# Optimization experiments

Measured on AMD Instinct MI355X. Metric: run time of the kernel, lower is better.

Reference implementation:

```python
import jax, jax.numpy as jnp
import numpy as np

NUM_HEADS = 12

def get_rel_pos(q_size, k_size, rel_pos):
    # q_size == k_size here; relative index = i - j + (k_size - 1)
    idx = jnp.arange(q_size)[:, None] - jnp.arange(k_size)[None, :] + (k_size - 1)
    return rel_pos[idx]  # (q_size, k_size, head_dim)


def setup_inputs() -> dict:
    key = jax.random.key(0)
    ks = jax.random.split(key, 7)
    B, H, W, C = 1, 64, 64, 768
    return {
        "x": jax.random.normal(ks[0], (B, H, W, C), jnp.float32),
        "w_qkv": jax.random.normal(ks[1], (C, 3 * C), jnp.float32) * 0.02,
        "b_qkv": jnp.zeros((3 * C,), jnp.float32),
        "w_o": jax.random.normal(ks[2], (C, C), jnp.float32) * 0.02,
        "b_o": jnp.zeros((C,), jnp.float32),
        "rel_pos_h": jax.random.normal(ks[3], (2 * H - 1, C // NUM_HEADS), jnp.float32) * 0.02,
        "rel_pos_w": jax.random.normal(ks[4], (2 * W - 1, C // NUM_HEADS), jnp.float32) * 0.02,
    }


def reference(x, w_qkv, b_qkv, w_o, b_o, rel_pos_h, rel_pos_w):
    B, H, W, C = x.shape
    NH = NUM_HEADS
    HD = C // NH
    scale = HD ** -0.5  # 0.125

    qkv = x @ w_qkv + b_qkv                                   # (B,H,W,3C)
    qkv = qkv.reshape(B, H * W, 3, NH, HD)
    qkv = jnp.transpose(qkv, (2, 0, 3, 1, 4)).reshape(3, B * NH, H * W, HD)
    q, k, v = qkv[0], qkv[1], qkv[2]                          # (B*NH, HW, HD)

    Rh = get_rel_pos(H, H, rel_pos_h)                         # (H,H,HD)
    Rw = get_rel_pos(W, W, rel_pos_w)                         # (W,W,HD)
    qr = q.reshape(B * NH, H, W, HD)
    rel_h = jnp.einsum('bhwc,hkc->bhwk', qr, Rh)              # (B*NH,H,W,H)
    rel_w = jnp.einsum('bhwc,wkc->bhwk', qr, Rw)              # (B*NH,H,W,W)

    attn = jnp.einsum('bmd,bnd->bmn', q, k) * scale           # (B*NH,HW,HW)
    attn = attn.reshape(B * NH, H, W, H, W)
    attn = attn + rel_h[:, :, :, :, None] + rel_w[:, :, :, None, :]
    attn = attn.reshape(B * NH, H * W, H * W)

    p = jax.nn.softmax(attn, axis=-1)
    o = jnp.einsum('bmn,bnd->bmd', p, v)                      # (B*NH,HW,HD)
    o = o.reshape(B, NH, H * W, HD)
    o = jnp.transpose(o, (0, 2, 1, 3)).reshape(B, H, W, C)    # heads concat in channel dim
    return o @ w_o + b_o
```

## Files before the change

### kernel.cpp

```cpp
#include <hip/hip_runtime.h>

#define DEVI __device__ __forceinline__
typedef unsigned short u16;
typedef unsigned int u32;
typedef __attribute__((ext_vector_type(4))) float f4v;
typedef __attribute__((ext_vector_type(8))) short bf8v;
typedef __attribute__((ext_vector_type(4))) u32  u32x4;
typedef __attribute__((ext_vector_type(2))) u32  u32x2;
typedef __attribute__((ext_vector_type(4))) u16  u16x4;

#define AS1 __attribute__((address_space(1)))
#define AS3 __attribute__((address_space(3)))

DEVI u16 f2bf(float x){ union{float f;u32 u;} c{x}; u32 r=(c.u+0x7FFFu+((c.u>>16)&1u))>>16; return (u16)r; }
DEVI float bf2f(u16 b){ union{u32 u;float f;} c{(u32)b<<16}; return c.f; }
DEVI f4v mfma32(bf8v a, bf8v b, f4v c){ return __builtin_amdgcn_mfma_f32_16x16x32_bf16(a,b,c,0,0,0); }
DEVI unsigned lds_off(const void* p){ return (unsigned)(unsigned long)(AS3 const void*)p; }
DEVI void glds16(const void* g, void* l){
  __builtin_amdgcn_global_load_lds((AS1 void*)g, (AS3 void*)l, 16, 0, 0);
}

static constexpr int NH = 12, HW = 4096, D = 64, C = 768;
static constexpr float LOG2E = 1.44269504f;

__global__ void qa_convx(const float* __restrict__ x, u16* __restrict__ xb, int n4){
  int i = blockIdx.x*256 + threadIdx.x;
  if(i >= n4) return;
  f4v v = ((const f4v*)x)[i];
  u16x4 o; for(int j=0;j<4;j++) o[j] = f2bf(v[j]);
  ((u16x4*)xb)[i] = o;
}

__global__ void qa_transp(const float* __restrict__ in, u16* __restrict__ out, int R, int Cc, int scale_k){
  __shared__ float tl[32][33];
  int t = threadIdx.x;
  int r0 = blockIdx.y*32, c0 = blockIdx.x*32;
  int tr = t>>3, tc = (t&7)*4;
  f4v v = *(const f4v*)&in[(r0+tr)*Cc + c0 + tc];
  for(int j=0;j<4;j++) tl[tr][tc+j] = v[j];
  __syncthreads();
  int oc = t>>3, orr = (t&7)*4;
  float sc = (scale_k && (c0+oc) >= 768 && (c0+oc) < 1536) ? 0.125f*LOG2E : 1.0f;
  u16x4 o; for(int j=0;j<4;j++) o[j] = f2bf(tl[orr+j][oc]*sc);
  *(u16x4*)&out[(c0+oc)*R + r0 + orr] = o;
}

__global__ __launch_bounds__(256,2) void qa_gemm_qkv(
    const u16* __restrict__ A, const u16* __restrict__ Bt, const float* __restrict__ bias,
    u16* __restrict__ qb, u16* __restrict__ kb, u16* __restrict__ vb){
  __shared__ u16 Al[128*32], Bl[128*32];
  const int t = threadIdx.x, lane = t&63, w = t>>6, c16 = lane&15, h4 = lane>>4;
  const int m0 = blockIdx.y*128, n0 = blockIdx.x*128;
  const int wr = w>>1, wc = w&1;
  f4v acc[4][4];
  for(int nt=0;nt<4;nt++){
    f4v bv;
    for(int r=0;r<4;r++){
      int col = n0 + wc*64 + nt*16 + 4*h4 + r;
      float b = bias[col];
      bv[r] = (col >= 768 && col < 1536) ? b*0.125f*LOG2E : b;
    }
    for(int mt=0;mt<4;mt++) acc[mt][nt] = bv;
  }
  for(int k0 = 0; k0 < 768; k0 += 32){
    __syncthreads();
    for(int i=0;i<2;i++){
      int off = i*4096 + w*1024 + lane*16;
      int row = off>>6, kk = (off&63)>>1;
      glds16(A  + (size_t)(m0+row)*768 + k0 + kk, (u16*)Al + i*2048 + w*512);
      glds16(Bt + (size_t)(n0+row)*768 + k0 + kk, (u16*)Bl + i*2048 + w*512);
    }
    __syncthreads();
    bf8v a[4], b[4];
    for(int mt=0;mt<4;mt++) a[mt] = *(const bf8v*)&Al[(wr*64+mt*16+c16)*32 + h4*8];
    for(int nt=0;nt<4;nt++) b[nt] = *(const bf8v*)&Bl[(wc*64+nt*16+c16)*32 + h4*8];
    for(int mt=0;mt<4;mt++) for(int nt=0;nt<4;nt++) acc[mt][nt] = mfma32(b[nt], a[mt], acc[mt][nt]);
  }
  for(int mt=0;mt<4;mt++){
    int row = m0 + wr*64 + mt*16 + c16;
    for(int nt=0;nt<4;nt++){
      int col0 = n0 + wc*64 + nt*16 + 4*h4;
      int which = col0/768, head = (col0>>6)%12, d0 = col0&63;
      u16* dst = which==0 ? qb : (which==1 ? kb : vb);
      u32x2 pk;
      asm("v_cvt_pk_bf16_f32 %0, %1, %2" : "=v"(pk[0]) : "v"(acc[mt][nt][0]), "v"(acc[mt][nt][1]));
      asm("v_cvt_pk_bf16_f32 %0, %1, %2" : "=v"(pk[1]) : "v"(acc[mt][nt][2]), "v"(acc[mt][nt][3]));
      *(u32x2*)&dst[((size_t)(head<<12)+row)*64 + d0] = pk;
    }
  }
}

__global__ __launch_bounds__(256) void qa_rel(
    const u16* __restrict__ qbuf, const float* __restrict__ rph, const float* __restrict__ rpw,
    u16* __restrict__ RHt, u16* __restrict__ RW){
  const int t = threadIdx.x, lane = t&63, w = t>>6, c16 = lane&15, h4 = lane>>4;
  const int qh = blockIdx.x, head = blockIdx.y;
  __shared__ u16 ql[64*72], hl[64*72], wl[128*72];
  {
    int row = t>>2, d0 = (t&3)*16;
    const u16* src = qbuf + ((size_t)(head<<12)+(qh<<6)+row)*64 + d0;
    *(u32x4*)&ql[row*72+d0]   = *(const u32x4*)src;
    *(u32x4*)&ql[row*72+d0+8] = *(const u32x4*)(src+8);
    for(int j=0;j<16;j++) hl[row*72+d0+j] = f2bf(rph[(qh+row)*64 + d0 + j]);
    int rw_r = t>>1, rd0 = (t&1)*32;
    for(int j=0;j<32;j++) wl[rw_r*72+rd0+j] = (rw_r<127) ? f2bf(rpw[rw_r*64+rd0+j]) : (u16)0;
  }
  __syncthreads();
  if(w < 2){
    bf8v a[2][2]; f4v acc[2][4] = {};
    for(int mt=0;mt<2;mt++) for(int ch=0;ch<2;ch++)
      a[mt][ch] = *(const bf8v*)&ql[(w*32+mt*16+c16)*72 + ch*32 + h4*8];
    for(int nt=0;nt<4;nt++) for(int ch=0;ch<2;ch++){
      bf8v b = *(const bf8v*)&hl[(nt*16+c16)*72 + ch*32 + h4*8];
      for(int mt=0;mt<2;mt++) acc[mt][nt] = mfma32(a[mt][ch], b, acc[mt][nt]);
    }
    for(int mt=0;mt<2;mt++) for(int nt=0;nt<4;nt++) for(int r=0;r<4;r++){
      int qw = w*32+mt*16+4*h4+r, c = nt*16+c16, kh = 63 - c;
      RHt[((size_t)(head*64+qh)*64+kh)*64 + qw] = f2bf(acc[mt][nt][r]*LOG2E);
    }
  } else {
    bf8v a[2][2]; f4v acc[2][8] = {};
    for(int mt=0;mt<2;mt++) for(int ch=0;ch<2;ch++)
      a[mt][ch] = *(const bf8v*)&ql[((w-2)*32+mt*16+c16)*72 + ch*32 + h4*8];
    for(int nt=0;nt<8;nt++) for(int ch=0;ch<2;ch++){
      bf8v b = *(const bf8v*)&wl[(nt*16+c16)*72 + ch*32 + h4*8];
      for(int mt=0;mt<2;mt++) acc[mt][nt] = mfma32(a[mt][ch], b, acc[mt][nt]);
    }
    for(int mt=0;mt<2;mt++) for(int nt=0;nt<8;nt++) for(int r=0;r<4;r++){
      int qw = (w-2)*32+mt*16+4*h4+r, c = nt*16+c16, kw = qw + 63 - c;
      if((unsigned)kw < 64u) RW[((size_t)(head*64+qh)*64+qw)*64 + kw] = f2bf(acc[mt][nt][r]*LOG2E);
    }
  }
}

__global__ __launch_bounds__(256,4) void qa_attn(
    const u16* __restrict__ qb, const u16* __restrict__ kb, const u16* __restrict__ vb,
    const u16* __restrict__ RHt, const u16* __restrict__ RW,
    u16* __restrict__ Op, float* __restrict__ Ps){
  __shared__ u16 Kl[2][4096];
  __shared__ u16 Vl[2][4096];
  __shared__ u16 RHl[2048];
  const int t = threadIdx.x, lane = t&63, w = t>>6, c16 = lane&15, h4 = lane>>4;
  const int bid = blockIdx.x;
  const int g = (bid&7)*192 + (bid>>3);
  const int s = g&1, unit = g>>1;
  const int head = unit>>6, qt = unit&63;

  const u16* rhg = RHt + (size_t)unit*4096 + s*2048;
  glds16(rhg + t*8, (u16*)RHl + w*512);

  int koff[2], voff[2];
  for(int i=0;i<2;i++){
    int u = i*256 + t;
    koff[i] = (u ^ ((u>>3)&7))*8;
    int key = ((u>>1)&3) | (((u>>3)&15)<<2);
    int d0  = ((u&1)<<3) | (((u>>7)&3)<<4);
    voff[i] = key*64 + d0;
  }
  const u16* kg = kb + (size_t)head*262144 + (size_t)s*32*4096;
  const u16* vg = vb + (size_t)head*262144 + (size_t)s*32*4096;
  const u16* kp = kg; const u16* vp = vg;
  for(int i=0;i<2;i++){
    glds16(kp + koff[i], (u16*)Kl[0] + (i*256 + w*64)*8);
    glds16(vp + voff[i], (u16*)Vl[0] + (i*256 + w*64)*8);
  }
  kp += 4096; vp += 4096;

  const int q0r = qt*64 + w*16;
  bf8v qa[2];
  {
    const u16* qsrc = qb + ((size_t)head*4096 + q0r + c16)*64;
    qa[0] = *(const bf8v*)(qsrc + h4*8);
    qa[1] = *(const bf8v*)(qsrc + 32 + h4*8);
  }
  float rw[4][4];
  for(int nt=0;nt<4;nt++) for(int r=0;r<4;r++){
    int qw = w*16 + c16, kw = nt*16 + 4*h4 + r;
    rw[nt][r] = bf2f(RW[((size_t)unit*64 + qw)*64 + kw]);
  }

  f4v oacc[4] = {}; f4v psv = {0.f,0.f,0.f,0.f};
  unsigned vcur = lds_off(Vl) + lane*8;
  const int kq0 = (h4*16) ^ ((c16&7)<<4);
  const int kq1 = (h4*16 + 64) ^ ((c16&7)<<4);
  const int kA  = c16*128;

  for(int it=0; it<32; it++){
    if(it == 31){ kp = kg; vp = vg; }
    {
      u16* Kn = (u16*)Kl[(it+1)&1]; u16* Vn = (u16*)Vl[(it+1)&1];
      for(int i=0;i<2;i++){
        glds16(kp + koff[i], Kn + (i*256 + w*64)*8);
        glds16(vp + voff[i], Vn + (i*256 + w*64)*8);
      }
    }
    kp += 4096; vp += 4096;
    asm volatile("s_waitcnt vmcnt(4)\n\ts_barrier" ::: "memory");

    const char* Kc = (const char*)Kl + (it&1)*8192;
    float rh = bf2f(RHl[it*64 + w*16 + c16]);
    f4v p[4];
    #pragma unroll
    for(int nt=0;nt<4;nt++){
      bf8v k0 = *(const bf8v*)(Kc + kA + nt*2048 + kq0);
      bf8v k1 = *(const bf8v*)(Kc + kA + nt*2048 + kq1);
      f4v sv;
      for(int r=0;r<4;r++) sv[r] = rh + rw[nt][r];
      __builtin_amdgcn_s_setprio(1);
      sv = mfma32(k0, qa[0], sv);
      sv = mfma32(k1, qa[1], sv);
      __builtin_amdgcn_s_setprio(0);
      f4v pe;
      for(int r=0;r<4;r++) pe[r] = __builtin_amdgcn_exp2f(sv[r]);
      p[nt] = pe;
      psv += pe;
    }
    union U8 { u32 w[4]; bf8v v; };
    U8 pb[2];
    #pragma unroll
    for(int half=0;half<2;half++)
      #pragma unroll
      for(int i=0;i<4;i++){
        int nt = half*2 + (i>>1), r0 = (i&1)*2;
        asm("v_cvt_pk_bf16_f32 %0, %1, %2"
            : "=v"(pb[half].w[i]) : "v"(p[nt][r0]), "v"(p[nt][r0+1]));
      }
    #pragma unroll
    for(int dt=0;dt<4;dt++){
      unsigned long t00,t01,t10,t11;
      asm volatile(
        "ds_read_b64_tr_b16 %0, %4 offset:%c5\n\t"
        "ds_read_b64_tr_b16 %1, %4 offset:%c6\n\t"
        "ds_read_b64_tr_b16 %2, %4 offset:%c7\n\t"
        "ds_read_b64_tr_b16 %3, %4 offset:%c8\n\t"
        "s_waitcnt lgkmcnt(0)"
        : "=&v"(t00), "=&v"(t01), "=&v"(t10), "=&v"(t11)
        : "v"(vcur), "i"(dt*2048), "i"(dt*2048+512), "i"(dt*2048+1024), "i"(dt*2048+1536)
        : "memory");
      union { struct{ unsigned long a,b; } q; bf8v v; } v01, v23;
      v01.q.a = t00; v01.q.b = t01; v23.q.a = t10; v23.q.b = t11;
      __builtin_amdgcn_s_setprio(1);
      oacc[dt] = mfma32(v01.v, pb[0].v, oacc[dt]);
      oacc[dt] = mfma32(v23.v, pb[1].v, oacc[dt]);
      __builtin_amdgcn_s_setprio(0);
    }
    asm volatile("s_waitcnt lgkmcnt(0)\n\ts_barrier" ::: "memory");
    vcur ^= 8192;
  }
  asm volatile("s_waitcnt vmcnt(0)" ::: "memory");

  {
    float v = psv[0]+psv[1]+psv[2]+psv[3];
    v += __shfl_xor(v, 16); v += __shfl_xor(v, 32);
    const int qrow_l = w*16 + c16;
    if(h4 == 0) Ps[((size_t)unit*2 + s)*64 + qrow_l] = v;
    const size_t obase = (((size_t)unit*2 + s)*64 + qrow_l)*64;
    #pragma unroll
    for(int dt=0;dt<4;dt++){
      u32x2 pk;
      asm("v_cvt_pk_bf16_f32 %0, %1, %2" : "=v"(pk[0]) : "v"(oacc[dt][0]), "v"(oacc[dt][1]));
      asm("v_cvt_pk_bf16_f32 %0, %1, %2" : "=v"(pk[1]) : "v"(oacc[dt][2]), "v"(oacc[dt][3]));
      *(u32x2*)&Op[obase + dt*16 + 4*h4] = pk;
    }
  }
}

__global__ __launch_bounds__(256) void qa_reduce(
    const u16* __restrict__ Op, const float* __restrict__ Ps, u16* __restrict__ ob){
  const int unit = blockIdx.x, t = threadIdx.x;
  const int head = unit>>6, qt = unit&63;
  const int d0 = (t&15)*4;
  #pragma unroll
  for(int qq=0;qq<4;qq++){
    int qr = (t>>4) + qq*16;
    float inv = 1.0f / (Ps[((size_t)unit*2)*64 + qr] + Ps[((size_t)unit*2+1)*64 + qr]);
    u16x4 a = *(const u16x4*)&Op[(((size_t)unit*2  )*64 + qr)*64 + d0];
    u16x4 b = *(const u16x4*)&Op[(((size_t)unit*2+1)*64 + qr)*64 + d0];
    u16x4 o;
    for(int j=0;j<4;j++) o[j] = f2bf((bf2f(a[j]) + bf2f(b[j]))*inv);
    *(u16x4*)&ob[(size_t)(qt*64 + qr)*768 + head*64 + d0] = o;
  }
}

__global__ __launch_bounds__(256,2) void qa_gemm_out(
    const u16* __restrict__ A, const u16* __restrict__ Bt, const float* __restrict__ bias,
    float* __restrict__ out){
  __shared__ u16 Al[128*32], Bl[128*32];
  const int t = threadIdx.x, lane = t&63, w = t>>6, c16 = lane&15, h4 = lane>>4;
  const int m0 = blockIdx.y*128, n0 = blockIdx.x*128;
  const int wr = w>>1, wc = w&1;
  f4v acc[4][4];
  for(int nt=0;nt<4;nt++){
    f4v bv = *(const f4v*)&bias[n0 + wc*64 + nt*16 + 4*h4];
    for(int mt=0;mt<4;mt++) acc[mt][nt] = bv;
  }
  for(int k0 = 0; k0 < 768; k0 += 32){
    __syncthreads();
    for(int i=0;i<2;i++){
      int off = i*4096 + w*1024 + lane*16;
      int row = off>>6, kk = (off&63)>>1;
      glds16(A  + (size_t)(m0+row)*768 + k0 + kk, (u16*)Al + i*2048 + w*512);
      glds16(Bt + (size_t)(n0+row)*768 + k0 + kk, (u16*)Bl + i*2048 + w*512);
    }
    __syncthreads();
    bf8v a[4], b[4];
    for(int mt=0;mt<4;mt++) a[mt] = *(const bf8v*)&Al[(wr*64+mt*16+c16)*32 + h4*8];
    for(int nt=0;nt<4;nt++) b[nt] = *(const bf8v*)&Bl[(wc*64+nt*16+c16)*32 + h4*8];
    for(int mt=0;mt<4;mt++) for(int nt=0;nt<4;nt++) acc[mt][nt] = mfma32(b[nt], a[mt], acc[mt][nt]);
  }
  for(int mt=0;mt<4;mt++){
    int row = m0 + wr*64 + mt*16 + c16;
    for(int nt=0;nt<4;nt++){
      int col0 = n0 + wc*64 + nt*16 + 4*h4;
      *(f4v*)&out[(size_t)row*768 + col0] = acc[mt][nt];
    }
  }
}

extern "C" void kernel_launch(void* const* d_in, const int* in_sizes, int n_in,
                              void* d_out, int out_size, void* d_ws, size_t ws_size,
                              hipStream_t stream){
  const float* x    = (const float*)d_in[0];
  const float* wqkv = (const float*)d_in[1];
  const float* bqkv = (const float*)d_in[2];
  const float* wo   = (const float*)d_in[3];
  const float* bo   = (const float*)d_in[4];
  const float* rph  = (const float*)d_in[5];
  const float* rpw  = (const float*)d_in[6];
  float* out = (float*)d_out;

  size_t off = 0;
  auto alloc = [&](size_t bytes){ void* p = (char*)d_ws + off; off += (bytes + 255) & ~(size_t)255; return p; };
  u16* x_bf   = (u16*)alloc((size_t)HW*C*2);
  u16* wqkv_t = (u16*)alloc((size_t)2304*768*2);
  u16* wo_t   = (u16*)alloc((size_t)768*768*2);
  u16* q_buf  = (u16*)alloc((size_t)NH*HW*D*2);
  u16* k_buf  = (u16*)alloc((size_t)NH*HW*D*2);
  u16* v_buf  = (u16*)alloc((size_t)NH*HW*D*2);
  u16* rh_buf = (u16*)alloc((size_t)NH*64*64*64*2);
  u16* rw_buf = (u16*)alloc((size_t)NH*64*64*64*2);
  u16* o_buf  = (u16*)alloc((size_t)HW*C*2);
  u16* op_buf = (u16*)alloc((size_t)768*2*64*64*2);
  float* ps_buf = (float*)alloc((size_t)768*2*64*4);

  int n4 = HW*C/4;
  qa_convx<<<(n4+255)/256, 256, 0, stream>>>(x, x_bf, n4);
  qa_transp<<<dim3(2304/32, 768/32), 256, 0, stream>>>(wqkv, wqkv_t, 768, 2304, 1);
  qa_transp<<<dim3(768/32, 768/32),  256, 0, stream>>>(wo,   wo_t,   768, 768, 0);
  qa_gemm_qkv<<<dim3(2304/128, HW/128), 256, 0, stream>>>(x_bf, wqkv_t, bqkv, q_buf, k_buf, v_buf);
  qa_rel<<<dim3(64, NH), 256, 0, stream>>>(q_buf, rph, rpw, rh_buf, rw_buf);
  qa_attn<<<1536, 256, 0, stream>>>(q_buf, k_buf, v_buf, rh_buf, rw_buf, op_buf, ps_buf);
  qa_reduce<<<768, 256, 0, stream>>>(op_buf, ps_buf, o_buf);
  qa_gemm_out<<<dim3(768/128, HW/128), 256, 0, stream>>>(o_buf, wo_t, bo, out);
}
```

Measured before the change: 154.9 us.

## Double the attention query tile to 128 rows per block

Each attention block now processes 128 query rows instead of 64, with every wave handling two 16-row query chunks against each shared K/V tile. This halves the K/V tile loads and barriers per unit of work and halves the grid size and partial-output buffers, with the reduce kernel adjusted to match. The cost is roughly double the accumulator and score registers per thread, so the occupancy target drops from 4 to 3 blocks per SM. There are also fewer blocks (768) to spread across the compute units.

New measurement: 144.1 us. -7.0%, faster.

```diff
diff --git a/kernel.cpp b/kernel.cpp
--- a/kernel.cpp
+++ b/kernel.cpp
@@ -133,32 +133,36 @@
   }
 }
 
-__global__ __launch_bounds__(256,4) void qa_attn(
+__global__ __launch_bounds__(256,3) void qa_attn(
     const u16* __restrict__ qb, const u16* __restrict__ kb, const u16* __restrict__ vb,
     const u16* __restrict__ RHt, const u16* __restrict__ RW,
     u16* __restrict__ Op, float* __restrict__ Ps){
   __shared__ u16 Kl[2][4096];
   __shared__ u16 Vl[2][4096];
-  __shared__ u16 RHl[2048];
+  __shared__ u16 RHl[4096];
   const int t = threadIdx.x, lane = t&63, w = t>>6, c16 = lane&15, h4 = lane>>4;
   const int bid = blockIdx.x;
-  const int g = (bid&7)*192 + (bid>>3);
-  const int s = g&1, unit = g>>1;
-  const int head = unit>>6, qt = unit&63;
-
-  const u16* rhg = RHt + (size_t)unit*4096 + s*2048;
-  glds16(rhg + t*8, (u16*)RHl + w*512);
+  const int g = (bid&7)*96 + (bid>>3);
+  const int s = g&1, u = g>>1;
+  const int head = u>>5, qblk = u&31;
+  const int B0 = qblk*128;
+  const int qhl = w>>1;
+
+  for(int i=0;i<2;i++){
+    const u16* rhsrc = RHt + (((size_t)(head*64 + qblk*2 + i))*64 + s*32)*64;
+    glds16(rhsrc + t*8, (u16*)RHl + i*2048 + w*512);
+  }
 
   int koff[2], voff[2];
   for(int i=0;i<2;i++){
-    int u = i*256 + t;
-    koff[i] = (u ^ ((u>>3)&7))*8;
-    int key = ((u>>1)&3) | (((u>>3)&15)<<2);
-    int d0  = ((u&1)<<3) | (((u>>7)&3)<<4);
+    int uu = i*256 + t;
+    koff[i] = (uu ^ ((uu>>3)&7))*8;
+    int key = ((uu>>1)&3) | (((uu>>3)&15)<<2);
+    int d0  = ((uu&1)<<3) | (((uu>>7)&3)<<4);
     voff[i] = key*64 + d0;
   }
-  const u16* kg = kb + (size_t)head*262144 + (size_t)s*32*4096;
-  const u16* vg = vb + (size_t)head*262144 + (size_t)s*32*4096;
+  const u16* kg = kb + (size_t)head*262144 + (size_t)s*131072;
+  const u16* vg = vb + (size_t)head*262144 + (size_t)s*131072;
   const u16* kp = kg; const u16* vp = vg;
   for(int i=0;i<2;i++){
     glds16(kp + koff[i], (u16*)Kl[0] + (i*256 + w*64)*8);
@@ -166,20 +170,20 @@
   }
   kp += 4096; vp += 4096;
 
-  const int q0r = qt*64 + w*16;
-  bf8v qa[2];
-  {
-    const u16* qsrc = qb + ((size_t)head*4096 + q0r + c16)*64;
-    qa[0] = *(const bf8v*)(qsrc + h4*8);
-    qa[1] = *(const bf8v*)(qsrc + 32 + h4*8);
-  }
-  float rw[4][4];
-  for(int nt=0;nt<4;nt++) for(int r=0;r<4;r++){
-    int qw = w*16 + c16, kw = nt*16 + 4*h4 + r;
-    rw[nt][r] = bf2f(RW[((size_t)unit*64 + qw)*64 + kw]);
-  }
-
-  f4v oacc[4] = {}; f4v psv = {0.f,0.f,0.f,0.f};
+  bf8v qa[2][2];
+  for(int qc=0;qc<2;qc++){
+    const u16* qsrc = qb + ((size_t)head*4096 + B0 + w*32 + qc*16 + c16)*64;
+    qa[qc][0] = *(const bf8v*)(qsrc + h4*8);
+    qa[qc][1] = *(const bf8v*)(qsrc + 32 + h4*8);
+  }
+  float rw[4][2][4];
+  for(int nt=0;nt<2*2;nt++);
+  for(int nt=0;nt<4;nt++) for(int qc=0;qc<2;qc++) for(int r=0;r<4;r++){
+    int qw = (w&1)*32 + qc*16 + c16, kw = nt*16 + 4*h4 + r;
+    rw[nt][qc][r] = bf2f(RW[(((size_t)(head*64 + qblk*2 + qhl))*64 + qw)*64 + kw]);
+  }
+
+  f4v oacc[4][2] = {}; f4v psv[2] = {};
   unsigned vcur = lds_off(Vl) + lane*8;
   const int kq0 = (h4*16) ^ ((c16&7)<<4);
   const int kq1 = (h4*16 + 64) ^ ((c16&7)<<4);
@@ -198,33 +202,40 @@
     asm volatile("s_waitcnt vmcnt(4)\n\ts_barrier" ::: "memory");
 
     const char* Kc = (const char*)Kl + (it&1)*8192;
-    float rh = bf2f(RHl[it*64 + w*16 + c16]);
-    f4v p[4];
+    float rh0 = bf2f(RHl[qhl*2048 + it*64 + (w&1)*32 + c16]);
+    float rh1 = bf2f(RHl[qhl*2048 + it*64 + (w&1)*32 + 16 + c16]);
+    f4v p[4][2];
     #pragma unroll
     for(int nt=0;nt<4;nt++){
       bf8v k0 = *(const bf8v*)(Kc + kA + nt*2048 + kq0);
       bf8v k1 = *(const bf8v*)(Kc + kA + nt*2048 + kq1);
-      f4v sv;
-      for(int r=0;r<4;r++) sv[r] = rh + rw[nt][r];
-      __builtin_amdgcn_s_setprio(1);
-      sv = mfma32(k0, qa[0], sv);
-      sv = mfma32(k1, qa[1], sv);
-      __builtin_amdgcn_s_setprio(0);
-      f4v pe;
-      for(int r=0;r<4;r++) pe[r] = __builtin_amdgcn_exp2f(sv[r]);
-      p[nt] = pe;
-      psv += pe;
+      #pragma unroll
+      for(int qc=0;qc<2;qc++){
+        f4v sv;
+        float rh = qc ? rh1 : rh0;
+        for(int r=0;r<4;r++) sv[r] = rh + rw[nt][qc][r];
+        __builtin_amdgcn_s_setprio(1);
+        sv = mfma32(k0, qa[qc][0], sv);
+        sv = mfma32(k1, qa[qc][1], sv);
+        __builtin_amdgcn_s_setprio(0);
+        f4v pe;
+        for(int r=0;r<4;r++) pe[r] = __builtin_amdgcn_exp2f(sv[r]);
+        p[nt][qc] = pe;
+        psv[qc] += pe;
+      }
     }
     union U8 { u32 w[4]; bf8v v; };
-    U8 pb[2];
+    U8 pb[2][2];
     #pragma unroll
     for(int half=0;half<2;half++)
       #pragma unroll
-      for(int i=0;i<4;i++){
-        int nt = half*2 + (i>>1), r0 = (i&1)*2;
-        asm("v_cvt_pk_bf16_f32 %0, %1, %2"
-            : "=v"(pb[half].w[i]) : "v"(p[nt][r0]), "v"(p[nt][r0+1]));
-      }
+      for(int qc=0;qc<2;qc++)
+        #pragma unroll
+        for(int i=0;i<4;i++){
+          int nt = half*2 + (i>>1), r0 = (i&1)*2;
+          asm("v_cvt_pk_bf16_f32 %0, %1, %2"
+              : "=v"(pb[half][qc].w[i]) : "v"(p[nt][qc][r0]), "v"(p[nt][qc][r0+1]));
+        }
     #pragma unroll
     for(int dt=0;dt<4;dt++){
       unsigned long t00,t01,t10,t11;
@@ -240,8 +251,11 @@
       union { struct{ unsigned long a,b; } q; bf8v v; } v01, v23;
       v01.q.a = t00; v01.q.b = t01; v23.q.a = t10; v23.q.b = t11;
       __builtin_amdgcn_s_setprio(1);
-      oacc[dt] = mfma32(v01.v, pb[0].v, oacc[dt]);
-      oacc[dt] = mfma32(v23.v, pb[1].v, oacc[dt]);
+      #pragma unroll
+      for(int qc=0;qc<2;qc++){
+        oacc[dt][qc] = mfma32(v01.v, pb[0][qc].v, oacc[dt][qc]);
+        oacc[dt][qc] = mfma32(v23.v, pb[1][qc].v, oacc[dt][qc]);
+      }
       __builtin_amdgcn_s_setprio(0);
     }
     asm volatile("s_waitcnt lgkmcnt(0)\n\ts_barrier" ::: "memory");
@@ -249,17 +263,18 @@
   }
   asm volatile("s_waitcnt vmcnt(0)" ::: "memory");
 
-  {
-    float v = psv[0]+psv[1]+psv[2]+psv[3];
+  #pragma unroll
+  for(int qc=0;qc<2;qc++){
+    float v = psv[qc][0]+psv[qc][1]+psv[qc][2]+psv[qc][3];
     v += __shfl_xor(v, 16); v += __shfl_xor(v, 32);
-    const int qrow_l = w*16 + c16;
-    if(h4 == 0) Ps[((size_t)unit*2 + s)*64 + qrow_l] = v;
-    const size_t obase = (((size_t)unit*2 + s)*64 + qrow_l)*64;
+    const int qrow_l = w*32 + qc*16 + c16;
+    if(h4 == 0) Ps[((size_t)u*2 + s)*128 + qrow_l] = v;
+    const size_t obase = (((size_t)u*2 + s)*128 + qrow_l)*64;
     #pragma unroll
     for(int dt=0;dt<4;dt++){
       u32x2 pk;
-      asm("v_cvt_pk_bf16_f32 %0, %1, %2" : "=v"(pk[0]) : "v"(oacc[dt][0]), "v"(oacc[dt][1]));
-      asm("v_cvt_pk_bf16_f32 %0, %1, %2" : "=v"(pk[1]) : "v"(oacc[dt][2]), "v"(oacc[dt][3]));
+      asm("v_cvt_pk_bf16_f32 %0, %1, %2" : "=v"(pk[0]) : "v"(oacc[dt][qc][0]), "v"(oacc[dt][qc][1]));
+      asm("v_cvt_pk_bf16_f32 %0, %1, %2" : "=v"(pk[1]) : "v"(oacc[dt][qc][2]), "v"(oacc[dt][qc][3]));
       *(u32x2*)&Op[obase + dt*16 + 4*h4] = pk;
     }
   }
@@ -267,18 +282,19 @@
 
 __global__ __launch_bounds__(256) void qa_reduce(
     const u16* __restrict__ Op, const float* __restrict__ Ps, u16* __restrict__ ob){
-  const int unit = blockIdx.x, t = threadIdx.x;
-  const int head = unit>>6, qt = unit&63;
+  const int u = blockIdx.x, t = threadIdx.x;
+  const int head = u>>5, qblk = u&31;
   const int d0 = (t&15)*4;
+  const size_t b0 = (size_t)u*2*128, b1 = b0 + 128;
   #pragma unroll
-  for(int qq=0;qq<4;qq++){
+  for(int qq=0;qq<8;qq++){
     int qr = (t>>4) + qq*16;
-    float inv = 1.0f / (Ps[((size_t)unit*2)*64 + qr] + Ps[((size_t)unit*2+1)*64 + qr]);
-    u16x4 a = *(const u16x4*)&Op[(((size_t)unit*2  )*64 + qr)*64 + d0];
-    u16x4 b = *(const u16x4*)&Op[(((size_t)unit*2+1)*64 + qr)*64 + d0];
+    float inv = 1.0f / (Ps[b0 + qr] + Ps[b1 + qr]);
+    u16x4 a = *(const u16x4*)&Op[(b0 + qr)*64 + d0];
+    u16x4 b = *(const u16x4*)&Op[(b1 + qr)*64 + d0];
     u16x4 o;
     for(int j=0;j<4;j++) o[j] = f2bf((bf2f(a[j]) + bf2f(b[j]))*inv);
-    *(u16x4*)&ob[(size_t)(qt*64 + qr)*768 + head*64 + d0] = o;
+    *(u16x4*)&ob[(size_t)(qblk*128 + qr)*768 + head*64 + d0] = o;
   }
 }
 
@@ -340,8 +356,8 @@
   u16* rh_buf = (u16*)alloc((size_t)NH*64*64*64*2);
   u16* rw_buf = (u16*)alloc((size_t)NH*64*64*64*2);
   u16* o_buf  = (u16*)alloc((size_t)HW*C*2);
-  u16* op_buf = (u16*)alloc((size_t)768*2*64*64*2);
-  float* ps_buf = (float*)alloc((size_t)768*2*64*4);
+  u16* op_buf = (u16*)alloc((size_t)384*2*128*64*2);
+  float* ps_buf = (float*)alloc((size_t)384*2*128*4);
 
   int n4 = HW*C/4;
   qa_convx<<<(n4+255)/256, 256, 0, stream>>>(x, x_bf, n4);
@@ -349,7 +365,7 @@
   qa_transp<<<dim3(768/32, 768/32),  256, 0, stream>>>(wo,   wo_t,   768, 768, 0);
   qa_gemm_qkv<<<dim3(2304/128, HW/128), 256, 0, stream>>>(x_bf, wqkv_t, bqkv, q_buf, k_buf, v_buf);
   qa_rel<<<dim3(64, NH), 256, 0, stream>>>(q_buf, rph, rpw, rh_buf, rw_buf);
-  qa_attn<<<1536, 256, 0, stream>>>(q_buf, k_buf, v_buf, rh_buf, rw_buf, op_buf, ps_buf);
-  qa_reduce<<<768, 256, 0, stream>>>(op_buf, ps_buf, o_buf);
+  qa_attn<<<768, 256, 0, stream>>>(q_buf, k_buf, v_buf, rh_buf, rw_buf, op_buf, ps_buf);
+  qa_reduce<<<384, 256, 0, stream>>>(op_buf, ps_buf, o_buf);
   qa_gemm_out<<<dim3(768/128, HW/128), 256, 0, stream>>>(o_buf, wo_t, bo, out);
 }
```
